# Optimization experiments

Hardware: AMD Instinct MI355X
Metric: run time of the kernel (lower is better)

The kernel has to match this reference:

```python
import jax, jax.numpy as jnp
import numpy as np
from jax import lax

KR = 2                      # kernel_radius
KS = 2 * KR + 1             # kernel_size = 5
ITER = 3                    # iter_time
THETA = jnp.float32(np.pi * 0.5)


def _sobel_kernels():
    # window_size=3, mult=2 -> classic Sobel (cross-correlation form)
    mx = np.zeros((3, 3), np.float32)
    my = np.zeros((3, 3), np.float32)
    for j in range(-1, 2):
        for i in range(-1, 2):
            d = float(i * i + j * j)
            if d != 0:
                mx[j + 1, i + 1] = 2.0 * i / d
                my[j + 1, i + 1] = 2.0 * j / d
    return jnp.asarray(mx), jnp.asarray(my)


def _grouped_conv(x, k2d):
    # x: (B,C,H,W); per-channel 3x3 cross-correlation, zero padding 1 (F.conv2d semantics)
    C = x.shape[1]
    kern = jnp.broadcast_to(k2d[None, None], (C, 1, 3, 3))
    return lax.conv_general_dilated(
        x, kern, window_strides=(1, 1), padding=[(1, 1), (1, 1)],
        feature_group_count=C, dimension_numbers=("NCHW", "OIHW", "NCHW"))


def _reflect_pad(x, r):
    return jnp.pad(x, ((0, 0), (0, 0), (r, r), (r, r)), mode="reflect")


def _patches(xpad, h, w):
    # xpad: (B,C,h+2r,w+2r) -> (B,C,h,w,KS,KS); static slices, KS*KS=25 views
    rows = []
    for i in range(KS):
        cols = [xpad[:, :, i:i + h, j:j + w] for j in range(KS)]
        rows.append(jnp.stack(cols, axis=-1))
    return jnp.stack(rows, axis=-2)  # (B,C,h,w,i,j)


def reference(img):
    B, C, h, w = img.shape
    img_n = img / jnp.amax(img, axis=(2, 3), keepdims=True)

    sx, sy = _sobel_kernels()
    gx = _grouped_conv(img_n, sx)
    gy = _grouped_conv(img_n, sy)
    # torch.clamp(min=1e-12): negatives are clipped up (faithful to source)
    gx = jnp.maximum(gx, 1e-12)
    gy = jnp.maximum(gy, 1e-12)

    gmag = jnp.sqrt(gx * gx + gy * gy)
    gnorm = gmag / jnp.amax(gmag, axis=(2, 3), keepdims=True)
    xn = gx / gmag
    yn = gy / gmag
    ct, st = jnp.cos(THETA), jnp.sin(THETA)  # fp32 rotation by pi/2
    xn, yn = xn * ct - yn * st, yn * ct + xn * st

    # Wm: 0.5*(1+tanh(eta*(neighbor_gradnorm - center_gradnorm))); Ws == 1
    g_nb = _patches(_reflect_pad(gnorm, KR), h, w)          # (B,C,h,w,k,k)
    Wm = 0.5 * (1.0 + jnp.tanh(g_nb - gnorm[..., None, None]))

    for _ in range(ITER):
        # Wd*phi == X.Y (abs * sign recombines exactly, incl. 0)
        Yx = _patches(_reflect_pad(xn, KR), h, w)
        Yy = _patches(_reflect_pad(yn, KR), h, w)
        dot = xn[..., None, None] * Yx + yn[..., None, None] * Yy
        kernels = Wm * dot                                   # phi*Ws*Wm*Wd

        mx = _patches(_reflect_pad(gnorm * xn, KR), h, w)
        my = _patches(_reflect_pad(gnorm * yn, KR), h, w)
        xr = jnp.sum(mx * kernels, axis=(-2, -1))
        yr = jnp.sum(my * kernels, axis=(-2, -1))
        mag = jnp.sqrt(xr * xr + yr * yr)
        xn = xr / mag
        yn = yr / mag

    angle = jnp.arctan(-yn / xn)
    a = 180.0 * angle / jnp.float32(np.pi)
    # F.instance_norm: per-(B,C) spatial standardization, biased var, eps=1e-5
    mean = jnp.mean(a, axis=(2, 3), keepdims=True)
    var = jnp.var(a, axis=(2, 3), keepdims=True)
    return (a - mean) / jnp.sqrt(var + 1e-5)


def setup_inputs() -> dict:
    key = jax.random.key(0)
    img = jax.random.uniform(key, (2, 3, 512, 512), dtype=jnp.float32)
    return {"img": img}
```

## Files before the change

kernel.cpp:

```cpp
#include <hip/hip_runtime.h>
#include <math.h>

#define H 512
#define W 512
#define HW (H * W)
#define NCH 6

__device__ __forceinline__ int reflect_idx(int p, int n) {
    if (p < 0) p = -p;
    if (p >= n) p = 2 * n - 2 - p;
    return p;
}

__global__ __launch_bounds__(256) void k_sobel(const float* __restrict__ img,
                                               float* __restrict__ gpart,
                                               float* __restrict__ g,
                                               float* __restrict__ xn,
                                               float* __restrict__ yn) {
    const int SW = 132, SH = 10;
    __shared__ float st[SH * SW];

    int ch = blockIdx.z;
    int bx0 = blockIdx.x * 128, by0 = blockIdx.y * 8;
    int tx = threadIdx.x, ty = threadIdx.y;
    int tid = ty * 32 + tx;
    const float* im = img + (size_t)ch * HW;

    for (int i = tid; i < SH * 130; i += 256) {
        int r = i / 130, c = i - r * 130;
        int yy = by0 - 1 + r, xx = bx0 - 1 + c;
        float v = 0.f;
        if (yy >= 0 && yy < H && xx >= 0 && xx < W) v = im[yy * W + xx];
        st[r * SW + c] = v;
    }
    __syncthreads();

    float bmax = 0.f;
    int y = by0 + ty;
    int r = ty + 1;
    float gm4[4], xr4[4], yr4[4];
#pragma unroll
    for (int k = 0; k < 4; ++k) {
        int c = tx + 32 * k + 1;
        float a00 = st[(r - 1) * SW + c - 1], a01 = st[(r - 1) * SW + c], a02 = st[(r - 1) * SW + c + 1];
        float a10 = st[r * SW + c - 1], a12 = st[r * SW + c + 1];
        float a20 = st[(r + 1) * SW + c - 1], a21 = st[(r + 1) * SW + c], a22 = st[(r + 1) * SW + c + 1];

        float gx = (a02 - a00) + 2.f * (a12 - a10) + (a22 - a20);
        float gy = (a20 - a00) + 2.f * (a21 - a01) + (a22 - a02);

        gx = fmaxf(gx, 1e-12f);
        gy = fmaxf(gy, 1e-12f);
        float d = gx * gx + gy * gy;
        float rq = __builtin_amdgcn_rsqf(d);
        float gm = d * rq;
        float xv = gx * rq, yv = gy * rq;
        const float ct = -4.37113883e-08f;
        gm4[k] = gm;
        xr4[k] = xv * ct - yv;
        yr4[k] = yv * ct + xv;
        bmax = fmaxf(bmax, gm);
    }
#pragma unroll
    for (int k = 0; k < 4; ++k) {
        int idx = y * W + bx0 + tx + 32 * k;
        float* gc = g + (size_t)ch * HW;
        float* xc = xn + (size_t)ch * HW;
        float* yc = yn + (size_t)ch * HW;
        gc[idx] = gm4[k];
        xc[idx] = xr4[k];
        yc[idx] = yr4[k];
    }

    __syncthreads();
    st[tid] = bmax;
    __syncthreads();
    for (int s = 128; s > 0; s >>= 1) {
        if (tid < s) st[tid] = fmaxf(st[tid], st[tid + s]);
        __syncthreads();
    }
    if (tid == 0) gpart[ch * 256 + blockIdx.y * 4 + blockIdx.x] = st[0];
}

template <bool LAST>
__global__ __launch_bounds__(256) void k_iter(const float* __restrict__ g,
                                              const float* __restrict__ xin,
                                              const float* __restrict__ yin,
                                              const float* __restrict__ gpart,
                                              float* __restrict__ xout,
                                              float* __restrict__ yout,
                                              double* __restrict__ partials) {
    const int SW = 136, SH = 12;
    __shared__ __align__(16) float sg[SH * SW];
    __shared__ __align__(16) float se[SH * SW];
    __shared__ __align__(16) float sx[SH * SW];
    __shared__ __align__(16) float sy[SH * SW];
    __shared__ float smax;

    int ch = blockIdx.z;
    int bx0 = blockIdx.x * 128, by0 = blockIdx.y * 8;
    int tx = threadIdx.x, ty = threadIdx.y;
    int tid = ty * 32 + tx;

    if (tid < 64) {
        const float* gp = gpart + ch * 256;
        float m = fmaxf(fmaxf(gp[tid], gp[tid + 64]), fmaxf(gp[tid + 128], gp[tid + 192]));
#pragma unroll
        for (int k = 32; k > 0; k >>= 1) m = fmaxf(m, __shfl_xor(m, k, 64));
        if (tid == 0) smax = m;
    }

    const float* gc = g + (size_t)ch * HW;
    const float* xc = xin + (size_t)ch * HW;
    const float* yc = yin + (size_t)ch * HW;
    float vg[7];
    int nj = 0;
    for (int i = tid; i < SH * 132; i += 256, ++nj) {
        int r = i / 132, c = i - r * 132;
        int yy = reflect_idx(by0 - 2 + r, H);
        int xx = reflect_idx(bx0 - 2 + c, W);
        int idx = yy * W + xx;
        int s = r * SW + c;
        float gv = gc[idx];
        vg[nj] = gv;
        sg[s] = gv;
        sx[s] = xc[idx];
        sy[s] = yc[idx];
    }
    __syncthreads();

    float inv = __builtin_amdgcn_rcpf(smax);
    float s2 = -2.f * inv;

    nj = 0;
    for (int i = tid; i < SH * 132; i += 256, ++nj) {
        int r = i / 132, c = i - r * 132;
        se[r * SW + c] = __expf(s2 * vg[nj]);
    }
    __syncthreads();

    auto ld8 = [&](const float* s, int r, float* w) {
        const float4* p = (const float4*)(s + r * SW + 4 * tx);
        float4 a = p[0], b = p[1];
        w[0] = a.x; w[1] = a.y; w[2] = a.z; w[3] = a.w;
        w[4] = b.x; w[5] = b.y; w[6] = b.z; w[7] = b.w;
    };

    int row0 = ty + 2;
    float cxw[8], cyw[8], cew[8];
    ld8(sx, row0, cxw);
    ld8(sy, row0, cyw);
    ld8(se, row0, cew);
    float cx[4], cy[4], ec[4];
#pragma unroll
    for (int k = 0; k < 4; ++k) {
        cx[k] = cxw[k + 2];
        cy[k] = cyw[k + 2];
        ec[k] = __builtin_amdgcn_rcpf(cew[k + 2]);
    }

    float xr[4] = {0.f, 0.f, 0.f, 0.f}, yr[4] = {0.f, 0.f, 0.f, 0.f};
#pragma unroll
    for (int dy = -2; dy <= 2; ++dy) {
        float gw[8], xw[8], yw[8], ew[8];
        ld8(sg, row0 + dy, gw);
        ld8(sx, row0 + dy, xw);
        ld8(sy, row0 + dy, yw);
        ld8(se, row0 + dy, ew);
#pragma unroll
        for (int k = 0; k < 4; ++k) {
#pragma unroll
            for (int dxi = 0; dxi < 5; ++dxi) {
                int n = k + dxi;
                float dot = cx[k] * xw[n] + cy[k] * yw[n];
                float wm = __builtin_amdgcn_rcpf(1.f + ew[n] * ec[k]);
                float m = gw[n] * (wm * dot);
                xr[k] = fmaf(m, xw[n], xr[k]);
                yr[k] = fmaf(m, yw[n], yr[k]);
            }
        }
    }

    int obase = (by0 + ty) * W + bx0 + 4 * tx;
    if (!LAST) {
        float* xo = xout + (size_t)ch * HW;
        float* yo = yout + (size_t)ch * HW;
        float ox[4], oy[4];
#pragma unroll
        for (int k = 0; k < 4; ++k) {
            float im2 = __builtin_amdgcn_rsqf(xr[k] * xr[k] + yr[k] * yr[k]);
            ox[k] = xr[k] * im2;
            oy[k] = yr[k] * im2;
        }
        *(float4*)(xo + obase) = make_float4(ox[0], ox[1], ox[2], ox[3]);
        *(float4*)(yo + obase) = make_float4(oy[0], oy[1], oy[2], oy[3]);
    } else {
        float a[4];
        double s = 0.0, q = 0.0;
#pragma unroll
        for (int k = 0; k < 4; ++k) {
            float ang = atanf(-yr[k] / xr[k]);
            a[k] = (180.f * ang) / 3.14159274f;
            s += (double)a[k];
            q += (double)a[k] * (double)a[k];
        }
        float* xo = xout + (size_t)ch * HW;
        *(float4*)(xo + obase) = make_float4(a[0], a[1], a[2], a[3]);

        __shared__ double rs[256], rq2[256];
        rs[tid] = s;
        rq2[tid] = q;
        __syncthreads();
        for (int st = 128; st > 0; st >>= 1) {
            if (tid < st) {
                rs[tid] += rs[tid + st];
                rq2[tid] += rq2[tid + st];
            }
            __syncthreads();
        }
        if (tid == 0) {
            int blk = blockIdx.y * 4 + blockIdx.x;
            partials[((size_t)ch * 256 + blk) * 2 + 0] = rs[0];
            partials[((size_t)ch * 256 + blk) * 2 + 1] = rq2[0];
        }
    }
}

__global__ __launch_bounds__(256) void k_norm(float* __restrict__ a,
                                              const double* __restrict__ partials) {
    int ch = blockIdx.y;
    int t = threadIdx.x;

    __shared__ double rs[256], rq[256];
    rs[t] = partials[((size_t)ch * 256 + t) * 2 + 0];
    rq[t] = partials[((size_t)ch * 256 + t) * 2 + 1];
    __syncthreads();
    for (int st = 128; st > 0; st >>= 1) {
        if (t < st) {
            rs[t] += rs[t + st];
            rq[t] += rq[t + st];
        }
        __syncthreads();
    }
    __shared__ float sm, ss;
    if (t == 0) {
        double mean = rs[0] / (double)HW;
        double var = rq[0] / (double)HW - mean * mean;
        sm = (float)mean;
        ss = (float)(1.0 / sqrt(var + 1e-5));
    }
    __syncthreads();
    float mean = sm, sc = ss;

    float4* a4 = (float4*)(a + (size_t)ch * HW + (size_t)blockIdx.x * 4096);
#pragma unroll
    for (int k = 0; k < 4; ++k) {
        float4 v = a4[k * 256 + t];
        v.x = (v.x - mean) * sc;
        v.y = (v.y - mean) * sc;
        v.z = (v.z - mean) * sc;
        v.w = (v.w - mean) * sc;
        a4[k * 256 + t] = v;
    }
}

extern "C" void kernel_launch(void* const* d_in, const int* in_sizes, int n_in,
                              void* d_out, int out_size, void* d_ws, size_t ws_size,
                              hipStream_t stream) {
    (void)in_sizes; (void)n_in; (void)out_size; (void)ws_size;
    const float* img = (const float*)d_in[0];
    float* out = (float*)d_out;

    float* wsf = (float*)d_ws;
    float* gpart = wsf + 512;
    double* partials = (double*)(wsf + 8192);
    float* g = wsf + 32768;
    float* xnA = g + (size_t)NCH * HW;
    float* ynA = xnA + (size_t)NCH * HW;
    float* xnB = ynA + (size_t)NCH * HW;
    float* ynB = xnB + (size_t)NCH * HW;

    dim3 tile_grid(4, 64, NCH), tile_blk(32, 8);

    k_sobel<<<tile_grid, tile_blk, 0, stream>>>(img, gpart, g, xnA, ynA);
    k_iter<false><<<tile_grid, tile_blk, 0, stream>>>(g, xnA, ynA, gpart, xnB, ynB, nullptr);
    k_iter<false><<<tile_grid, tile_blk, 0, stream>>>(g, xnB, ynB, gpart, xnA, ynA, nullptr);
    k_iter<true><<<tile_grid, tile_blk, 0, stream>>>(g, xnA, ynA, gpart, out, nullptr, partials);
    k_norm<<<dim3(64, NCH), dim3(256), 0, stream>>>(out, partials);
}
```

Before: 132.4 us.

## Fuse three ETF iterations into one kernel with halo recompute in LDS

Replaces the three separate iteration launches with a single kernel that loads a 64x16 tile plus a 6-pixel halo into shared memory. It runs the first two iterations on shrinking regions in place, then the final one with the angle and partial-sum output. This removes two kernel launches and the global round trips of the intermediate x/y fields. In exchange it recomputes the halo region, which adds redundant arithmetic, and uses smaller tiles with more shared memory per block.

```diff
diff --git a/kernel.cpp b/kernel.cpp
--- a/kernel.cpp
+++ b/kernel.cpp
@@ -82,75 +82,32 @@
     if (tid == 0) gpart[ch * 256 + blockIdx.y * 4 + blockIdx.x] = st[0];
 }
 
-template <bool LAST>
-__global__ __launch_bounds__(256) void k_iter(const float* __restrict__ g,
-                                              const float* __restrict__ xin,
-                                              const float* __restrict__ yin,
-                                              const float* __restrict__ gpart,
-                                              float* __restrict__ xout,
-                                              float* __restrict__ yout,
-                                              double* __restrict__ partials) {
-    const int SW = 136, SH = 12;
-    __shared__ __align__(16) float sg[SH * SW];
-    __shared__ __align__(16) float se[SH * SW];
-    __shared__ __align__(16) float sx[SH * SW];
-    __shared__ __align__(16) float sy[SH * SW];
-    __shared__ float smax;
-
-    int ch = blockIdx.z;
-    int bx0 = blockIdx.x * 128, by0 = blockIdx.y * 8;
-    int tx = threadIdx.x, ty = threadIdx.y;
-    int tid = ty * 32 + tx;
-
-    if (tid < 64) {
-        const float* gp = gpart + ch * 256;
-        float m = fmaxf(fmaxf(gp[tid], gp[tid + 64]), fmaxf(gp[tid + 128], gp[tid + 192]));
-#pragma unroll
-        for (int k = 32; k > 0; k >>= 1) m = fmaxf(m, __shfl_xor(m, k, 64));
-        if (tid == 0) smax = m;
-    }
-
-    const float* gc = g + (size_t)ch * HW;
-    const float* xc = xin + (size_t)ch * HW;
-    const float* yc = yin + (size_t)ch * HW;
-    float vg[7];
-    int nj = 0;
-    for (int i = tid; i < SH * 132; i += 256, ++nj) {
-        int r = i / 132, c = i - r * 132;
-        int yy = reflect_idx(by0 - 2 + r, H);
-        int xx = reflect_idx(bx0 - 2 + c, W);
-        int idx = yy * W + xx;
-        int s = r * SW + c;
-        float gv = gc[idx];
-        vg[nj] = gv;
-        sg[s] = gv;
-        sx[s] = xc[idx];
-        sy[s] = yc[idx];
-    }
-    __syncthreads();
-
-    float inv = __builtin_amdgcn_rcpf(smax);
-    float s2 = -2.f * inv;
-
-    nj = 0;
-    for (int i = tid; i < SH * 132; i += 256, ++nj) {
-        int r = i / 132, c = i - r * 132;
-        se[r * SW + c] = __expf(s2 * vg[nj]);
-    }
-    __syncthreads();
-
-    auto ld8 = [&](const float* s, int r, float* w) {
-        const float4* p = (const float4*)(s + r * SW + 4 * tx);
-        float4 a = p[0], b = p[1];
+#define ST 80
+#define SR 28
+#define SC 76
+
+template <int OFF>
+__device__ __forceinline__ void ldrow(const float* p, float* w) {
+    const float4* q = (const float4*)p;
+    float4 a = q[0], b = q[1];
+    if (OFF == 0) {
         w[0] = a.x; w[1] = a.y; w[2] = a.z; w[3] = a.w;
         w[4] = b.x; w[5] = b.y; w[6] = b.z; w[7] = b.w;
-    };
-
-    int row0 = ty + 2;
+    } else {
+        float4 c = q[2];
+        w[0] = a.z; w[1] = a.w; w[2] = b.x; w[3] = b.y;
+        w[4] = b.z; w[5] = b.w; w[6] = c.x; w[7] = c.y;
+    }
+}
+
+template <int OFF>
+__device__ __forceinline__ void etf_group(const float* sg, const float* se,
+                                          const float* sx, const float* sy,
+                                          int row, int ab, float* xr, float* yr) {
     float cxw[8], cyw[8], cew[8];
-    ld8(sx, row0, cxw);
-    ld8(sy, row0, cyw);
-    ld8(se, row0, cew);
+    ldrow<OFF>(sx + row * ST + ab, cxw);
+    ldrow<OFF>(sy + row * ST + ab, cyw);
+    ldrow<OFF>(se + row * ST + ab, cew);
     float cx[4], cy[4], ec[4];
 #pragma unroll
     for (int k = 0; k < 4; ++k) {
@@ -158,15 +115,16 @@
         cy[k] = cyw[k + 2];
         ec[k] = __builtin_amdgcn_rcpf(cew[k + 2]);
     }
-
-    float xr[4] = {0.f, 0.f, 0.f, 0.f}, yr[4] = {0.f, 0.f, 0.f, 0.f};
+#pragma unroll
+    for (int k = 0; k < 4; ++k) { xr[k] = 0.f; yr[k] = 0.f; }
 #pragma unroll
     for (int dy = -2; dy <= 2; ++dy) {
         float gw[8], xw[8], yw[8], ew[8];
-        ld8(sg, row0 + dy, gw);
-        ld8(sx, row0 + dy, xw);
-        ld8(sy, row0 + dy, yw);
-        ld8(se, row0 + dy, ew);
+        const int rb = (row + dy) * ST + ab;
+        ldrow<OFF>(sg + rb, gw);
+        ldrow<OFF>(sx + rb, xw);
+        ldrow<OFF>(sy + rb, yw);
+        ldrow<OFF>(se + rb, ew);
 #pragma unroll
         for (int k = 0; k < 4; ++k) {
 #pragma unroll
@@ -180,21 +138,105 @@
             }
         }
     }
-
-    int obase = (by0 + ty) * W + bx0 + 4 * tx;
-    if (!LAST) {
-        float* xo = xout + (size_t)ch * HW;
-        float* yo = yout + (size_t)ch * HW;
-        float ox[4], oy[4];
+}
+
+template <int X0, int Y0, int WW, int HH>
+__device__ __forceinline__ void run_phase(const float* sg, const float* se,
+                                          float* sx, float* sy, int tid) {
+    constexpr int W4 = WW / 4;
+    constexpr int SB = ((X0 - 2) / 4) * 4;
+    constexpr int OFF = (X0 - 2) - SB;
+    constexpr int NG = W4 * HH;
+    float ox[2][4], oy[2][4];
+    int ng = 0;
+    for (int gi = tid; gi < NG; gi += 256, ++ng) {
+        int gm = gi % W4, gr = gi / W4;
+        int row = Y0 + gr;
+        int ab = SB + 4 * gm;
+        float xr[4], yr[4];
+        etf_group<OFF>(sg, se, sx, sy, row, ab, xr, yr);
 #pragma unroll
         for (int k = 0; k < 4; ++k) {
             float im2 = __builtin_amdgcn_rsqf(xr[k] * xr[k] + yr[k] * yr[k]);
-            ox[k] = xr[k] * im2;
-            oy[k] = yr[k] * im2;
-        }
-        *(float4*)(xo + obase) = make_float4(ox[0], ox[1], ox[2], ox[3]);
-        *(float4*)(yo + obase) = make_float4(oy[0], oy[1], oy[2], oy[3]);
-    } else {
+            ox[ng][k] = xr[k] * im2;
+            oy[ng][k] = yr[k] * im2;
+        }
+    }
+    __syncthreads();
+    ng = 0;
+    for (int gi = tid; gi < NG; gi += 256, ++ng) {
+        int gm = gi % W4, gr = gi / W4;
+        int c0 = (Y0 + gr) * ST + X0 + 4 * gm;
+        *(float2*)&sx[c0] = make_float2(ox[ng][0], ox[ng][1]);
+        *(float2*)&sx[c0 + 2] = make_float2(ox[ng][2], ox[ng][3]);
+        *(float2*)&sy[c0] = make_float2(oy[ng][0], oy[ng][1]);
+        *(float2*)&sy[c0 + 2] = make_float2(oy[ng][2], oy[ng][3]);
+    }
+    __syncthreads();
+}
+
+__global__ __launch_bounds__(256) void k_fused3(const float* __restrict__ g,
+                                                const float* __restrict__ xin,
+                                                const float* __restrict__ yin,
+                                                const float* __restrict__ gpart,
+                                                float* __restrict__ out,
+                                                double* __restrict__ partials) {
+    __shared__ __align__(16) float sg[SR * ST];
+    __shared__ __align__(16) float se[SR * ST];
+    __shared__ __align__(16) float sx[SR * ST];
+    __shared__ __align__(16) float sy[SR * ST];
+    __shared__ float smax;
+    __shared__ double rs[256], rq[256];
+
+    int ch = blockIdx.z;
+    int bx0 = blockIdx.x * 64, by0 = blockIdx.y * 16;
+    int tid = threadIdx.x;
+
+    if (tid < 64) {
+        const float* gp = gpart + ch * 256;
+        float m = fmaxf(fmaxf(gp[tid], gp[tid + 64]), fmaxf(gp[tid + 128], gp[tid + 192]));
+#pragma unroll
+        for (int k = 32; k > 0; k >>= 1) m = fmaxf(m, __shfl_xor(m, k, 64));
+        if (tid == 0) smax = m;
+    }
+
+    const float* gc = g + (size_t)ch * HW;
+    const float* xc = xin + (size_t)ch * HW;
+    const float* yc = yin + (size_t)ch * HW;
+    float vg[9];
+    int nj = 0;
+    for (int i = tid; i < SR * SC; i += 256, ++nj) {
+        int r = i / SC, c = i - r * SC;
+        int yy = reflect_idx(by0 - 6 + r, H);
+        int xx = reflect_idx(bx0 - 6 + c, W);
+        int idx = yy * W + xx;
+        int s = r * ST + c;
+        float gv = gc[idx];
+        vg[nj] = gv;
+        sg[s] = gv;
+        sx[s] = xc[idx];
+        sy[s] = yc[idx];
+    }
+    __syncthreads();
+
+    float s2 = -2.f * __builtin_amdgcn_rcpf(smax);
+    nj = 0;
+    for (int i = tid; i < SR * SC; i += 256, ++nj) {
+        int r = i / SC, c = i - r * SC;
+        se[r * ST + c] = __expf(s2 * vg[nj]);
+    }
+    __syncthreads();
+
+    run_phase<2, 2, 72, 24>(sg, se, sx, sy, tid);
+    run_phase<4, 4, 68, 20>(sg, se, sx, sy, tid);
+
+    {
+        int gm = tid & 15, gr = tid >> 4;
+        int row = 6 + gr;
+        int ab = 4 + 4 * gm;
+        float xr[4], yr[4];
+        etf_group<0>(sg, se, sx, sy, row, ab, xr, yr);
+
         float a[4];
         double s = 0.0, q = 0.0;
 #pragma unroll
@@ -204,25 +246,24 @@
             s += (double)a[k];
             q += (double)a[k] * (double)a[k];
         }
-        float* xo = xout + (size_t)ch * HW;
-        *(float4*)(xo + obase) = make_float4(a[0], a[1], a[2], a[3]);
-
-        __shared__ double rs[256], rq2[256];
+        float* oc = out + (size_t)ch * HW;
+        *(float4*)(oc + (by0 + gr) * W + bx0 + 4 * gm) = make_float4(a[0], a[1], a[2], a[3]);
+
         rs[tid] = s;
-        rq2[tid] = q;
+        rq[tid] = q;
+    }
+    __syncthreads();
+    for (int st = 128; st > 0; st >>= 1) {
+        if (tid < st) {
+            rs[tid] += rs[tid + st];
+            rq[tid] += rq[tid + st];
+        }
         __syncthreads();
-        for (int st = 128; st > 0; st >>= 1) {
-            if (tid < st) {
-                rs[tid] += rs[tid + st];
-                rq2[tid] += rq2[tid + st];
-            }
-            __syncthreads();
-        }
-        if (tid == 0) {
-            int blk = blockIdx.y * 4 + blockIdx.x;
-            partials[((size_t)ch * 256 + blk) * 2 + 0] = rs[0];
-            partials[((size_t)ch * 256 + blk) * 2 + 1] = rq2[0];
-        }
+    }
+    if (tid == 0) {
+        int blk = blockIdx.y * 8 + blockIdx.x;
+        partials[((size_t)ch * 256 + blk) * 2 + 0] = rs[0];
+        partials[((size_t)ch * 256 + blk) * 2 + 1] = rq[0];
     }
 }
 
@@ -277,14 +318,8 @@
     float* g = wsf + 32768;
     float* xnA = g + (size_t)NCH * HW;
     float* ynA = xnA + (size_t)NCH * HW;
-    float* xnB = ynA + (size_t)NCH * HW;
-    float* ynB = xnB + (size_t)NCH * HW;
-
-    dim3 tile_grid(4, 64, NCH), tile_blk(32, 8);
-
-    k_sobel<<<tile_grid, tile_blk, 0, stream>>>(img, gpart, g, xnA, ynA);
-    k_iter<false><<<tile_grid, tile_blk, 0, stream>>>(g, xnA, ynA, gpart, xnB, ynB, nullptr);
-    k_iter<false><<<tile_grid, tile_blk, 0, stream>>>(g, xnB, ynB, gpart, xnA, ynA, nullptr);
-    k_iter<true><<<tile_grid, tile_blk, 0, stream>>>(g, xnA, ynA, gpart, out, nullptr, partials);
+
+    k_sobel<<<dim3(4, 64, NCH), dim3(32, 8), 0, stream>>>(img, gpart, g, xnA, ynA);
+    k_fused3<<<dim3(8, 32, NCH), dim3(256), 0, stream>>>(g, xnA, ynA, gpart, out, partials);
     k_norm<<<dim3(64, NCH), dim3(256), 0, stream>>>(out, partials);
 }
```

New measurement: 153.5 us. 1.16x slower.

## Restructure halo loads, hoist channel max into a separate kernel, use shuffle reductions

Applied to the files above, without the earlier changes.

Replaces the div/mod-indexed tile loads in the Sobel and iteration kernels with row-structured loops that avoid integer division. The exp weight is now computed during the load, which removes a second pass and one barrier. The per-block reduction of the channel max moves into a tiny separate kernel, and the double-precision block sum in the last iteration becomes wavefront shuffles. This trims per-block overhead and barriers at the cost of one extra small launch.

```diff
diff --git a/kernel.cpp b/kernel.cpp
--- a/kernel.cpp
+++ b/kernel.cpp
@@ -17,8 +17,8 @@
                                                float* __restrict__ g,
                                                float* __restrict__ xn,
                                                float* __restrict__ yn) {
-    const int SW = 132, SH = 10;
-    __shared__ float st[SH * SW];
+    const int SW = 132;
+    __shared__ float st[10 * SW];
 
     int ch = blockIdx.z;
     int bx0 = blockIdx.x * 128, by0 = blockIdx.y * 8;
@@ -26,12 +26,29 @@
     int tid = ty * 32 + tx;
     const float* im = img + (size_t)ch * HW;
 
-    for (int i = tid; i < SH * 130; i += 256) {
-        int r = i / 130, c = i - r * 130;
-        int yy = by0 - 1 + r, xx = bx0 - 1 + c;
-        float v = 0.f;
-        if (yy >= 0 && yy < H && xx >= 0 && xx < W) v = im[yy * W + xx];
-        st[r * SW + c] = v;
+#pragma unroll
+    for (int jr = 0; jr < 2; ++jr) {
+        int r = ty + 8 * jr;
+        if (jr == 0 || ty < 2) {
+            int yy = by0 - 1 + r;
+            bool yok = (yy >= 0 && yy < H);
+            const float* rowp = im + yy * W;
+#pragma unroll
+            for (int m = 0; m < 4; ++m) {
+                int c = tx + 32 * m;
+                int xx = bx0 - 1 + c;
+                float v = 0.f;
+                if (yok && xx >= 0 && xx < W) v = rowp[xx];
+                st[r * SW + c] = v;
+            }
+            if (tx < 2) {
+                int c = 128 + tx;
+                int xx = bx0 - 1 + c;
+                float v = 0.f;
+                if (yok && xx >= 0 && xx < W) v = rowp[xx];
+                st[r * SW + c] = v;
+            }
+        }
     }
     __syncthreads();
 
@@ -82,109 +99,110 @@
     if (tid == 0) gpart[ch * 256 + blockIdx.y * 4 + blockIdx.x] = st[0];
 }
 
+__global__ __launch_bounds__(64) void k_red(const float* __restrict__ gpart,
+                                            float* __restrict__ gmax) {
+    int ch = blockIdx.x;
+    int t = threadIdx.x;
+    const float* gp = gpart + ch * 256;
+    float m = fmaxf(fmaxf(gp[t], gp[t + 64]), fmaxf(gp[t + 128], gp[t + 192]));
+#pragma unroll
+    for (int k = 32; k > 0; k >>= 1) m = fmaxf(m, __shfl_xor(m, k, 64));
+    if (t == 0) gmax[ch] = m;
+}
+
+struct W8 { float w[8]; };
+
 template <bool LAST>
 __global__ __launch_bounds__(256) void k_iter(const float* __restrict__ g,
                                               const float* __restrict__ xin,
                                               const float* __restrict__ yin,
-                                              const float* __restrict__ gpart,
+                                              const float* __restrict__ gmaxp,
                                               float* __restrict__ xout,
                                               float* __restrict__ yout,
                                               double* __restrict__ partials) {
-    const int SW = 136, SH = 12;
-    __shared__ __align__(16) float sg[SH * SW];
-    __shared__ __align__(16) float se[SH * SW];
-    __shared__ __align__(16) float sx[SH * SW];
-    __shared__ __align__(16) float sy[SH * SW];
-    __shared__ float smax;
+    const int SW = 136;
+    __shared__ __align__(16) float sg[12 * SW];
+    __shared__ __align__(16) float se[12 * SW];
+    __shared__ __align__(16) float sx[12 * SW];
+    __shared__ __align__(16) float sy[12 * SW];
+    __shared__ double swr[8];
 
     int ch = blockIdx.z;
     int bx0 = blockIdx.x * 128, by0 = blockIdx.y * 8;
     int tx = threadIdx.x, ty = threadIdx.y;
     int tid = ty * 32 + tx;
-
-    if (tid < 64) {
-        const float* gp = gpart + ch * 256;
-        float m = fmaxf(fmaxf(gp[tid], gp[tid + 64]), fmaxf(gp[tid + 128], gp[tid + 192]));
-#pragma unroll
-        for (int k = 32; k > 0; k >>= 1) m = fmaxf(m, __shfl_xor(m, k, 64));
-        if (tid == 0) smax = m;
-    }
-
-    const float* gc = g + (size_t)ch * HW;
-    const float* xc = xin + (size_t)ch * HW;
-    const float* yc = yin + (size_t)ch * HW;
-    float vg[7];
-    int nj = 0;
-    for (int i = tid; i < SH * 132; i += 256, ++nj) {
-        int r = i / 132, c = i - r * 132;
-        int yy = reflect_idx(by0 - 2 + r, H);
-        int xx = reflect_idx(bx0 - 2 + c, W);
-        int idx = yy * W + xx;
-        int s = r * SW + c;
-        float gv = gc[idx];
-        vg[nj] = gv;
-        sg[s] = gv;
-        sx[s] = xc[idx];
-        sy[s] = yc[idx];
-    }
-    __syncthreads();
-
-    float inv = __builtin_amdgcn_rcpf(smax);
-    float s2 = -2.f * inv;
-
-    nj = 0;
-    for (int i = tid; i < SH * 132; i += 256, ++nj) {
-        int r = i / 132, c = i - r * 132;
-        se[r * SW + c] = __expf(s2 * vg[nj]);
-    }
-    __syncthreads();
-
-    auto ld8 = [&](const float* s, int r, float* w) {
+    const size_t cbase = (size_t)ch * HW;
+
+    float s2 = -2.f * __builtin_amdgcn_rcpf(gmaxp[ch]);
+
+    const float* gc = g + cbase;
+    const float* xc = xin + cbase;
+    const float* yc = yin + cbase;
+#pragma unroll
+    for (int jr = 0; jr < 2; ++jr) {
+        int r = ty + 8 * jr;
+        if (jr == 0 || ty < 4) {
+            int yy = reflect_idx(by0 - 2 + r, H);
+            const float* grow = gc + yy * W;
+            const float* xrow = xc + yy * W;
+            const float* yrow = yc + yy * W;
+#pragma unroll
+            for (int m = 0; m < 5; ++m) {
+                int c = (m < 4) ? (tx + 32 * m) : (128 + tx);
+                if (m < 4 || tx < 4) {
+                    int xx = reflect_idx(bx0 - 2 + c, W);
+                    int s = r * SW + c;
+                    float gv = grow[xx];
+                    sg[s] = gv;
+                    se[s] = __expf(s2 * gv);
+                    sx[s] = xrow[xx];
+                    sy[s] = yrow[xx];
+                }
+            }
+        }
+    }
+    __syncthreads();
+
+    auto LD8 = [&](const float* s, int r) {
+        W8 o;
         const float4* p = (const float4*)(s + r * SW + 4 * tx);
         float4 a = p[0], b = p[1];
-        w[0] = a.x; w[1] = a.y; w[2] = a.z; w[3] = a.w;
-        w[4] = b.x; w[5] = b.y; w[6] = b.z; w[7] = b.w;
+        o.w[0] = a.x; o.w[1] = a.y; o.w[2] = a.z; o.w[3] = a.w;
+        o.w[4] = b.x; o.w[5] = b.y; o.w[6] = b.z; o.w[7] = b.w;
+        return o;
     };
 
     int row0 = ty + 2;
-    float cxw[8], cyw[8], cew[8];
-    ld8(sx, row0, cxw);
-    ld8(sy, row0, cyw);
-    ld8(se, row0, cew);
+    W8 cxw = LD8(sx, row0), cyw = LD8(sy, row0), cew = LD8(se, row0);
     float cx[4], cy[4], ec[4];
 #pragma unroll
     for (int k = 0; k < 4; ++k) {
-        cx[k] = cxw[k + 2];
-        cy[k] = cyw[k + 2];
-        ec[k] = __builtin_amdgcn_rcpf(cew[k + 2]);
+        cx[k] = cxw.w[k + 2];
+        cy[k] = cyw.w[k + 2];
+        ec[k] = __builtin_amdgcn_rcpf(cew.w[k + 2]);
     }
 
     float xr[4] = {0.f, 0.f, 0.f, 0.f}, yr[4] = {0.f, 0.f, 0.f, 0.f};
 #pragma unroll
     for (int dy = -2; dy <= 2; ++dy) {
-        float gw[8], xw[8], yw[8], ew[8];
-        ld8(sg, row0 + dy, gw);
-        ld8(sx, row0 + dy, xw);
-        ld8(sy, row0 + dy, yw);
-        ld8(se, row0 + dy, ew);
+        W8 gw = LD8(sg, row0 + dy), xw = LD8(sx, row0 + dy),
+           yw = LD8(sy, row0 + dy), ew = LD8(se, row0 + dy);
 #pragma unroll
         for (int k = 0; k < 4; ++k) {
 #pragma unroll
             for (int dxi = 0; dxi < 5; ++dxi) {
                 int n = k + dxi;
-                float dot = cx[k] * xw[n] + cy[k] * yw[n];
-                float wm = __builtin_amdgcn_rcpf(1.f + ew[n] * ec[k]);
-                float m = gw[n] * (wm * dot);
-                xr[k] = fmaf(m, xw[n], xr[k]);
-                yr[k] = fmaf(m, yw[n], yr[k]);
+                float dot = cx[k] * xw.w[n] + cy[k] * yw.w[n];
+                float wm = __builtin_amdgcn_rcpf(1.f + ew.w[n] * ec[k]);
+                float m = gw.w[n] * (wm * dot);
+                xr[k] = fmaf(m, xw.w[n], xr[k]);
+                yr[k] = fmaf(m, yw.w[n], yr[k]);
             }
         }
     }
 
-    int obase = (by0 + ty) * W + bx0 + 4 * tx;
+    size_t obase = cbase + (size_t)(by0 + ty) * W + bx0 + 4 * tx;
     if (!LAST) {
-        float* xo = xout + (size_t)ch * HW;
-        float* yo = yout + (size_t)ch * HW;
         float ox[4], oy[4];
 #pragma unroll
         for (int k = 0; k < 4; ++k) {
@@ -192,8 +210,8 @@
             ox[k] = xr[k] * im2;
             oy[k] = yr[k] * im2;
         }
-        *(float4*)(xo + obase) = make_float4(ox[0], ox[1], ox[2], ox[3]);
-        *(float4*)(yo + obase) = make_float4(oy[0], oy[1], oy[2], oy[3]);
+        *(float4*)(xout + obase) = make_float4(ox[0], ox[1], ox[2], ox[3]);
+        *(float4*)(yout + obase) = make_float4(oy[0], oy[1], oy[2], oy[3]);
     } else {
         float a[4];
         double s = 0.0, q = 0.0;
@@ -204,24 +222,24 @@
             s += (double)a[k];
             q += (double)a[k] * (double)a[k];
         }
-        float* xo = xout + (size_t)ch * HW;
-        *(float4*)(xo + obase) = make_float4(a[0], a[1], a[2], a[3]);
-
-        __shared__ double rs[256], rq2[256];
-        rs[tid] = s;
-        rq2[tid] = q;
+        *(float4*)(xout + obase) = make_float4(a[0], a[1], a[2], a[3]);
+
+#pragma unroll
+        for (int off = 32; off > 0; off >>= 1) {
+            s += __shfl_down(s, off, 64);
+            q += __shfl_down(q, off, 64);
+        }
+        if ((tid & 63) == 0) {
+            swr[tid >> 6] = s;
+            swr[4 + (tid >> 6)] = q;
+        }
         __syncthreads();
-        for (int st = 128; st > 0; st >>= 1) {
-            if (tid < st) {
-                rs[tid] += rs[tid + st];
-                rq2[tid] += rq2[tid + st];
-            }
-            __syncthreads();
-        }
         if (tid == 0) {
+            double ts = swr[0] + swr[1] + swr[2] + swr[3];
+            double tq = swr[4] + swr[5] + swr[6] + swr[7];
             int blk = blockIdx.y * 4 + blockIdx.x;
-            partials[((size_t)ch * 256 + blk) * 2 + 0] = rs[0];
-            partials[((size_t)ch * 256 + blk) * 2 + 1] = rq2[0];
+            partials[((size_t)ch * 256 + blk) * 2 + 0] = ts;
+            partials[((size_t)ch * 256 + blk) * 2 + 1] = tq;
         }
     }
 }
@@ -272,6 +290,7 @@
     float* out = (float*)d_out;
 
     float* wsf = (float*)d_ws;
+    float* gmax = wsf + 8;
     float* gpart = wsf + 512;
     double* partials = (double*)(wsf + 8192);
     float* g = wsf + 32768;
@@ -283,8 +302,9 @@
     dim3 tile_grid(4, 64, NCH), tile_blk(32, 8);
 
     k_sobel<<<tile_grid, tile_blk, 0, stream>>>(img, gpart, g, xnA, ynA);
-    k_iter<false><<<tile_grid, tile_blk, 0, stream>>>(g, xnA, ynA, gpart, xnB, ynB, nullptr);
-    k_iter<false><<<tile_grid, tile_blk, 0, stream>>>(g, xnB, ynB, gpart, xnA, ynA, nullptr);
-    k_iter<true><<<tile_grid, tile_blk, 0, stream>>>(g, xnA, ynA, gpart, out, nullptr, partials);
+    k_red<<<dim3(NCH), dim3(64), 0, stream>>>(gpart, gmax);
+    k_iter<false><<<tile_grid, tile_blk, 0, stream>>>(g, xnA, ynA, gmax, xnB, ynB, nullptr);
+    k_iter<false><<<tile_grid, tile_blk, 0, stream>>>(g, xnB, ynB, gmax, xnA, ynA, nullptr);
+    k_iter<true><<<tile_grid, tile_blk, 0, stream>>>(g, xnA, ynA, gmax, out, nullptr, partials);
     k_norm<<<dim3(64, NCH), dim3(256), 0, stream>>>(out, partials);
 }
```

Measured after the change: 124.6 us. 1.06x faster.
